# Kernel tuning notes

Measured on AMD Instinct MI355X. Metric: run time of the kernel, lower is better.

## Reference

```python
import jax, jax.numpy as jnp
import numpy as np

N_NODES = 50000
N_EDGES = 800000
D_IN = 128
D_HID = 128
D_OUT = 128
N_LAYERS = 2
NEG_SLOPE = 0.2


def leaky(x):
    return jnp.where(x >= 0, x, NEG_SLOPE * x)


def setup_inputs() -> dict:
    key = jax.random.key(0)
    ks = jax.random.split(key, 12)
    s = 1.0 / np.sqrt(D_HID)
    feats = jax.random.normal(ks[0], (N_NODES, D_IN), dtype=jnp.float32)
    src = jax.random.randint(ks[1], (N_EDGES,), 0, N_NODES)
    dst = jax.random.randint(ks[2], (N_EDGES,), 0, N_NODES)
    # SIRConv params per layer: W_Q (dst), W_K (src), W_R (output proj)
    Wq = jax.random.normal(ks[3], (N_LAYERS, D_IN, D_HID), dtype=jnp.float32) * s
    bq = jnp.zeros((N_LAYERS, D_HID), dtype=jnp.float32)
    Wk = jax.random.normal(ks[4], (N_LAYERS, D_IN, D_HID), dtype=jnp.float32) * s
    bk = jnp.zeros((N_LAYERS, D_HID), dtype=jnp.float32)
    Wr = jax.random.normal(ks[5], (N_LAYERS, D_HID, D_HID), dtype=jnp.float32) * s
    br = jnp.zeros((N_LAYERS, D_HID), dtype=jnp.float32)
    # Jumping-knowledge readouts: one per entry of feats_list (input + each layer);
    # input_dim == hidden_dim so weights stack along the leading axis.
    Wro = jax.random.normal(ks[6], (N_LAYERS + 1, D_HID, D_OUT), dtype=jnp.float32) * s
    bro = jnp.zeros((N_LAYERS + 1, D_OUT), dtype=jnp.float32)
    return {"feats": feats, "Wq": Wq, "bq": bq, "Wk": Wk, "bk": bk,
            "Wr": Wr, "br": br, "Wro": Wro, "bro": bro,
            "src": src, "dst": dst}


def reference(feats, Wq, bq, Wk, bk, Wr, br, Wro, bro, src, dst):
    # mean-aggregation denominator: in-degree, clamped to 1
    deg = jax.ops.segment_sum(jnp.ones((N_EDGES,), jnp.float32), dst,
                              num_segments=N_NODES)
    denom = jnp.maximum(deg, 1.0)[:, None]  # [N, 1]

    feats_list = [feats]
    h = feats
    for i in range(N_LAYERS):
        hq = h @ Wq[i] + bq[i]          # [N, H] (dst transform)
        hk = h @ Wk[i] + bk[i]          # [N, H] (src transform)
        m = leaky(hq[dst] + hk[src])    # [E, H] contextualized messages
        agg = jax.ops.segment_sum(m, dst, num_segments=N_NODES) / denom
        h = agg @ Wr[i] + br[i]         # conv output (+ residual = 0)
        h = leaky(h)                    # norm='none', dropout=0
        feats_list.append(h)

    # jumping-knowledge readout: sum of per-stage linear readouts
    score = feats_list[0] @ Wro[0] + bro[0]
    for i in range(1, N_LAYERS + 1):
        score = score + feats_list[i] @ Wro[i] + bro[i]
    return score
```

## Files before the change

kernel.cpp:

```cpp
#include <hip/hip_runtime.h>

#define NN 50000
#define NE 800000
#define D 128
#define NEG 0.2f

#define NBLK1 256
#define TILE1 3125
#define NB2 196
#define CAP2 8192
#define NT64 782

#define SB_PREP 576
#define SB_CONV 6250
#define SB_HIST NBLK1
#define SB_TOTAL (SB_PREP + SB_CONV + SB_HIST)

typedef short bf8_t __attribute__((ext_vector_type(8)));
typedef float f4_t __attribute__((ext_vector_type(4)));

__device__ __forceinline__ unsigned short f2bf(float f) {
  unsigned int u = __float_as_uint(f);
  return (unsigned short)((u + 0x7FFF + ((u >> 16) & 1)) >> 16);
}
__device__ __forceinline__ float bf2f(unsigned int b) { return __uint_as_float(b << 16); }

__device__ __forceinline__ f4_t MF(bf8_t a, bf8_t b, f4_t c) {
  return __builtin_amdgcn_mfma_f32_16x16x32_bf16(a, b, c, 0, 0, 0);
}

__device__ __forceinline__ int swz_u(int u) { return u ^ ((u >> 4) & 7); }


__device__ __forceinline__ void stage_wh(unsigned short* wbuf,
                                         const unsigned short* __restrict__ WTh, int t) {
#pragma unroll
  for (int i = 0; i < 4; ++i) {
    int u = t + i * 256;
    *(uint4*)(wbuf + swz_u(u) * 8) = *(const uint4*)(WTh + u * 8);
  }
}

__device__ __forceinline__ void load_a16(const unsigned short* __restrict__ A,
                                         int base, int l15, int quad, bf8_t (&afr)[4]) {
  int r = base + l15;
  if (r >= NN) r = NN - 1;
  const unsigned short* p = A + (size_t)r * D + quad * 8;
#pragma unroll
  for (int kc = 0; kc < 4; ++kc) afr[kc] = *(const bf8_t*)(p + kc * 32);
}

__device__ __forceinline__ void load_a16_lds(const unsigned short* buf, int wave,
                                             int l15, int quad, bf8_t (&afr)[4]) {
  const int r = wave * 16 + l15;
#pragma unroll
  for (int kc = 0; kc < 4; ++kc)
    afr[kc] = *(const bf8_t*)(buf + swz_u(r * 16 + kc * 4 + quad) * 8);
}

__device__ __forceinline__ void tile16h(const unsigned short* wbuf, const bf8_t (&afr)[4],
                                        int l15, int quad, f4_t* acc4) {
#pragma unroll
  for (int kc = 0; kc < 4; ++kc)
#pragma unroll
    for (int nt = 0; nt < 4; ++nt) {
      bf8_t b = *(const bf8_t*)(wbuf + swz_u((nt * 16 + l15) * 16 + kc * 4 + quad) * 8);
      acc4[nt] = MF(afr[kc], b, acc4[nt]);
    }
}

__device__ __forceinline__ void store_c8(unsigned short* __restrict__ C,
                                         const float* __restrict__ bias,
                                         const f4_t (&acc)[8], int base, int l15,
                                         int quad, bool lk) {
#pragma unroll
  for (int j = 0; j < 8; ++j) {
    int col = (j >> 2) * 64 + (j & 3) * 16 + l15;
    float bb = bias[col];
#pragma unroll
    for (int reg = 0; reg < 4; ++reg) {
      int row = base + quad * 4 + reg;
      if (row < NN) {
        float v = acc[j][reg] + bb;
        if (lk) v = v >= 0.f ? v : NEG * v;
        C[(size_t)row * D + col] = f2bf(v);
      }
    }
  }
}

#define ACC_TO_ABUF(ACC, BIAS)                                        \
  {                                                                   \
    _Pragma("unroll") for (int j = 0; j < 8; ++j) {                   \
      int col = (j >> 2) * 64 + (j & 3) * 16 + l15;                   \
      float bb = (BIAS)[col];                                         \
      _Pragma("unroll") for (int reg = 0; reg < 4; ++reg) {           \
        int rl = wave * 16 + quad * 4 + reg;                          \
        float v = ACC[j][reg] + bb;                                   \
        v = v >= 0.f ? v : NEG * v;                                   \
        int s = rl * D + col;                                         \
        abuf[s ^ ((rl & 7) << 3)] = f2bf(v);                          \
      }                                                               \
    }                                                                 \
  }

__global__ __launch_bounds__(256) void setup(
    const float* __restrict__ Wq, const float* __restrict__ Wk,
    const float* __restrict__ Wr, const float* __restrict__ Wro,
    const float* __restrict__ feats, const int* __restrict__ dst,
    unsigned short* __restrict__ WT, unsigned short* __restrict__ x0,
    int* __restrict__ H) {
  __shared__ int cnt[NB2];
  const int b = blockIdx.x;
  const int t = threadIdx.x;
  if (b < SB_PREP) {
    const int m = b >> 6, xb = b & 63;
    const float* src;
    if (m < 2) src = Wq + m * D * D;
    else if (m < 4) src = Wk + (m - 2) * D * D;
    else if (m < 6) src = Wr + (m - 4) * D * D;
    else src = Wro + (m - 6) * D * D;
    const int n = xb * 2 + (t >> 7);
    const int k = t & 127;
    WT[(size_t)m * D * D + n * D + k] = f2bf(src[k * D + n]);
  } else if (b < SB_PREP + SB_CONV) {
    int i = ((b - SB_PREP) * 256 + t) * 4;
    float4 v = *(const float4*)(feats + i);
    ushort4 o = {f2bf(v.x), f2bf(v.y), f2bf(v.z), f2bf(v.w)};
    *(ushort4*)(x0 + i) = o;
  } else {
    const int blk = b - SB_PREP - SB_CONV;
    if (t < NB2) cnt[t] = 0;
    __syncthreads();
    const int beg = blk * TILE1, end = beg + TILE1;
    for (int i = beg + t; i < end; i += 256) atomicAdd(&cnt[dst[i] >> 8], 1);
    __syncthreads();
    if (t < NB2) H[t * NBLK1 + blk] = cnt[t];
  }
}

__global__ __launch_bounds__(256) void p1_scan(const int* __restrict__ H,
                                               int* __restrict__ gofs) {
  __shared__ int sd[256];
  __shared__ int wsum[4];
  const int bin = blockIdx.x;
  const int t = threadIdx.x;
  const int wave = t >> 6, lane = t & 63;
  int part = 0;
  for (int b2 = 0; b2 < bin; ++b2) part += H[b2 * NBLK1 + t];
  for (int off = 32; off; off >>= 1) part += __shfl_down(part, off, 64);
  if (lane == 0) wsum[wave] = part;
  __syncthreads();
  const int base = wsum[0] + wsum[1] + wsum[2] + wsum[3];
  int x = H[bin * NBLK1 + t];
  sd[t] = x;
  __syncthreads();
  int acc = x;
  for (int off = 1; off < 256; off <<= 1) {
    int y = (t >= off) ? sd[t - off] : 0;
    __syncthreads();
    acc += y;
    sd[t] = acc;
    __syncthreads();
  }
  gofs[bin * NBLK1 + t] = base + (acc - x);
}

__global__ __launch_bounds__(256) void p1_scatter(const int* __restrict__ src,
                                                  const int* __restrict__ dst,
                                                  const int* __restrict__ gofs,
                                                  unsigned int* __restrict__ ebuf) {
  __shared__ int lofs[NB2];
  const int t = threadIdx.x;
  const int blk = blockIdx.x;
  if (t < NB2) lofs[t] = gofs[t * NBLK1 + blk];
  __syncthreads();
  const int beg = blk * TILE1, end = beg + TILE1;
  for (int i = beg + t; i < end; i += 256) {
    unsigned int d = (unsigned int)dst[i];
    int pos = atomicAdd(&lofs[d >> 8], 1);
    ebuf[pos] = (unsigned int)src[i] | (d << 16);
  }
}

__global__ __launch_bounds__(256) void sort_qk0(
    const int* __restrict__ gofs, const unsigned int* __restrict__ ebuf,
    int* __restrict__ ssrc, int* __restrict__ rowptr, int* __restrict__ deg,
    const unsigned short* __restrict__ x0,
    const unsigned short* __restrict__ WTq, const float* __restrict__ bq_,
    const unsigned short* __restrict__ WTk, const float* __restrict__ bk_,
    unsigned short* __restrict__ hq, unsigned short* __restrict__ hk) {
  __shared__ __align__(16) unsigned char smraw[35840];
  const int t = threadIdx.x;
  const int gx = blockIdx.x;
  if (gx < NB2) {
    int* cnt = (int*)smraw;
    int* fill = cnt + 256;
    int* sd = fill + 256;
    unsigned int* sorted = (unsigned int*)(sd + 256);
    const int b = gx;
    const int beg = gofs[b * NBLK1];
    const int end = (b + 1 < NB2) ? gofs[(b + 1) * NBLK1] : NE;
    const int n = end - beg;
    cnt[t] = 0;
    __syncthreads();
    for (int i = beg + t; i < end; i += 256)
      atomicAdd(&cnt[(ebuf[i] >> 16) & 255], 1);
    __syncthreads();
    int x = cnt[t];
    sd[t] = x;
    __syncthreads();
    int acc = x;
    for (int off = 1; off < 256; off <<= 1) {
      int y = (t >= off) ? sd[t - off] : 0;
      __syncthreads();
      acc += y;
      sd[t] = acc;
      __syncthreads();
    }
    const int excl = acc - x;
    fill[t] = excl;
    __syncthreads();
    for (int i = beg + t; i < end; i += 256) {
      unsigned int p = ebuf[i];
      int pos = atomicAdd(&fill[(p >> 16) & 255], 1);
      if (pos < CAP2) sorted[pos] = p;
    }
    __syncthreads();
    for (int i = t; i < n; i += 256) ssrc[beg + i] = (int)(sorted[i] & 0xFFFFu);
    const int node = (b << 8) + t;
    if (node < NN) {
      rowptr[node] = beg + excl;
      deg[node] = x;
    }
    if (b == 0 && t == 0) rowptr[NN] = NE;
  } else {
    unsigned short* wbuf = (unsigned short*)smraw;
    const int tile = gx - NB2;
    const int wave = t >> 6, lane = t & 63;
    const int l15 = lane & 15, quad = lane >> 4;
    const int base = tile * 64 + wave * 16;
    bf8_t afr[4];
    load_a16(x0, base, l15, quad, afr);
    stage_wh(wbuf, WTq, t);
    __syncthreads();
    f4_t aq[8] = {};
    tile16h(wbuf, afr, l15, quad, aq);
    __syncthreads();
    stage_wh(wbuf, WTq + 64 * D, t);
    __syncthreads();
    tile16h(wbuf, afr, l15, quad, aq + 4);
    store_c8(hq, bq_, aq, base, l15, quad, false);
    __syncthreads();
    stage_wh(wbuf, WTk, t);
    __syncthreads();
    f4_t ak[8] = {};
    tile16h(wbuf, afr, l15, quad, ak);
    __syncthreads();
    stage_wh(wbuf, WTk + 64 * D, t);
    __syncthreads();
    tile16h(wbuf, afr, l15, quad, ak + 4);
    store_c8(hk, bk_, ak, base, l15, quad, false);
  }
}

#define PROC(kb)                                                     \
  {                                                                  \
    float m;                                                         \
    m = q[0] + bf2f(kb.x & 0xFFFFu); a[0] += m >= 0.f ? m : NEG * m; \
    m = q[1] + bf2f(kb.x >> 16);     a[1] += m >= 0.f ? m : NEG * m; \
    m = q[2] + bf2f(kb.y & 0xFFFFu); a[2] += m >= 0.f ? m : NEG * m; \
    m = q[3] + bf2f(kb.y >> 16);     a[3] += m >= 0.f ? m : NEG * m; \
    m = q[4] + bf2f(kb.z & 0xFFFFu); a[4] += m >= 0.f ? m : NEG * m; \
    m = q[5] + bf2f(kb.z >> 16);     a[5] += m >= 0.f ? m : NEG * m; \
    m = q[6] + bf2f(kb.w & 0xFFFFu); a[6] += m >= 0.f ? m : NEG * m; \
    m = q[7] + bf2f(kb.w >> 16);     a[7] += m >= 0.f ? m : NEG * m; \
  }

__global__ __launch_bounds__(256) void aggregate(
    const int* __restrict__ rowptr, const int* __restrict__ ssrc,
    const int* __restrict__ deg,
    const unsigned short* __restrict__ hq, const unsigned short* __restrict__ hk,
    unsigned short* __restrict__ ag) {
  const int wave = threadIdx.x >> 6, lane = threadIdx.x & 63;
  const int v = blockIdx.x * 4 + wave;
  if (v >= NN) return;
  const int sub = lane & 15, grp = lane >> 4;
  const int beg = rowptr[v], end = rowptr[v + 1];

  uint4 qb = *(const uint4*)(hq + (size_t)v * D + sub * 8);
  float q[8];
  q[0] = bf2f(qb.x & 0xFFFFu); q[1] = bf2f(qb.x >> 16);
  q[2] = bf2f(qb.y & 0xFFFFu); q[3] = bf2f(qb.y >> 16);
  q[4] = bf2f(qb.z & 0xFFFFu); q[5] = bf2f(qb.z >> 16);
  q[6] = bf2f(qb.w & 0xFFFFu); q[7] = bf2f(qb.w >> 16);

  float a[8] = {0.f, 0.f, 0.f, 0.f, 0.f, 0.f, 0.f, 0.f};
  int e = beg + grp;
  for (; e + 12 < end; e += 16) {
    int s0 = ssrc[e];
    int s1 = ssrc[e + 4];
    int s2 = ssrc[e + 8];
    int s3 = ssrc[e + 12];
    uint4 k0 = *(const uint4*)(hk + (size_t)s0 * D + sub * 8);
    uint4 k1 = *(const uint4*)(hk + (size_t)s1 * D + sub * 8);
    uint4 k2 = *(const uint4*)(hk + (size_t)s2 * D + sub * 8);
    uint4 k3 = *(const uint4*)(hk + (size_t)s3 * D + sub * 8);
    PROC(k0);
    PROC(k1);
    PROC(k2);
    PROC(k3);
  }
  for (; e + 4 < end; e += 8) {
    int s0 = ssrc[e];
    int s1 = ssrc[e + 4];
    uint4 k0 = *(const uint4*)(hk + (size_t)s0 * D + sub * 8);
    uint4 k1 = *(const uint4*)(hk + (size_t)s1 * D + sub * 8);
    PROC(k0);
    PROC(k1);
  }
  if (e < end) {
    int s0 = ssrc[e];
    uint4 k0 = *(const uint4*)(hk + (size_t)s0 * D + sub * 8);
    PROC(k0);
  }
#pragma unroll
  for (int j = 0; j < 8; ++j) {
    a[j] += __shfl_xor(a[j], 16, 64);
    a[j] += __shfl_xor(a[j], 32, 64);
  }
  if (grp == 0) {
    float inv = 1.f / fmaxf((float)deg[v], 1.f);
    uint4 o;
    o.x = (unsigned int)f2bf(a[0] * inv) | ((unsigned int)f2bf(a[1] * inv) << 16);
    o.y = (unsigned int)f2bf(a[2] * inv) | ((unsigned int)f2bf(a[3] * inv) << 16);
    o.z = (unsigned int)f2bf(a[4] * inv) | ((unsigned int)f2bf(a[5] * inv) << 16);
    o.w = (unsigned int)f2bf(a[6] * inv) | ((unsigned int)f2bf(a[7] * inv) << 16);
    *(uint4*)(ag + (size_t)v * D + sub * 8) = o;
  }
}

__global__ __launch_bounds__(256) void wr_qk1(
    const unsigned short* __restrict__ ag,
    const unsigned short* __restrict__ WTr, const float* __restrict__ brr,
    unsigned short* __restrict__ h1,
    const unsigned short* __restrict__ WTq, const float* __restrict__ bq1,
    unsigned short* __restrict__ hq,
    const unsigned short* __restrict__ WTk, const float* __restrict__ bk1,
    unsigned short* __restrict__ hk) {
  __shared__ unsigned short wbuf[64 * D];
  __shared__ unsigned short abuf[64 * D];
  const int t = threadIdx.x, wave = t >> 6, lane = t & 63;
  const int l15 = lane & 15, quad = lane >> 4;
  const int tb = blockIdx.x * 64;
  const int base = tb + wave * 16;

  bf8_t afr[4];
  load_a16(ag, base, l15, quad, afr);
  stage_wh(wbuf, WTr, t);
  __syncthreads();
  f4_t acc[8] = {};
  tile16h(wbuf, afr, l15, quad, acc);
  __syncthreads();
  stage_wh(wbuf, WTr + 64 * D, t);
  __syncthreads();
  tile16h(wbuf, afr, l15, quad, acc + 4);

  ACC_TO_ABUF(acc, brr);
  __syncthreads();

  bf8_t hfr[4];
  load_a16_lds(abuf, wave, l15, quad, hfr);
#pragma unroll
  for (int i = 0; i < 4; ++i) {
    int u = t + i * 256;
    int row = tb + (u >> 4);
    if (row < NN)
      *(uint4*)(h1 + (size_t)tb * D + u * 8) = *(const uint4*)(abuf + swz_u(u) * 8);
  }

  stage_wh(wbuf, WTq, t);
  __syncthreads();
  f4_t aq[8] = {};
  tile16h(wbuf, hfr, l15, quad, aq);
  __syncthreads();
  stage_wh(wbuf, WTq + 64 * D, t);
  __syncthreads();
  tile16h(wbuf, hfr, l15, quad, aq + 4);
  store_c8(hq, bq1, aq, base, l15, quad, false);
  __syncthreads();

  stage_wh(wbuf, WTk, t);
  __syncthreads();
  f4_t ak[8] = {};
  tile16h(wbuf, hfr, l15, quad, ak);
  __syncthreads();
  stage_wh(wbuf, WTk + 64 * D, t);
  __syncthreads();
  tile16h(wbuf, hfr, l15, quad, ak + 4);
  store_c8(hk, bk1, ak, base, l15, quad, false);
}

__global__ __launch_bounds__(256) void wr_ro(
    const unsigned short* __restrict__ ag,
    const unsigned short* __restrict__ WTr, const float* __restrict__ brr,
    const unsigned short* __restrict__ x0,
    const unsigned short* __restrict__ h1,
    const unsigned short* __restrict__ WTro, const float* __restrict__ bro_,
    float* __restrict__ out) {
  __shared__ unsigned short wbuf[64 * D];
  __shared__ unsigned short abuf[64 * D];
  const int t = threadIdx.x, wave = t >> 6, lane = t & 63;
  const int l15 = lane & 15, quad = lane >> 4;
  const int tb = blockIdx.x * 64;
  const int base = tb + wave * 16;
  const size_t WM = (size_t)D * D;

  bf8_t afr[4];
  load_a16(ag, base, l15, quad, afr);
  stage_wh(wbuf, WTr, t);
  __syncthreads();
  f4_t acch[8] = {};
  tile16h(wbuf, afr, l15, quad, acch);
  __syncthreads();
  stage_wh(wbuf, WTr + 64 * D, t);
  __syncthreads();
  tile16h(wbuf, afr, l15, quad, acch + 4);

  ACC_TO_ABUF(acch, brr);
  __syncthreads();

  bf8_t hfr[4];
  load_a16_lds(abuf, wave, l15, quad, hfr);
  f4_t acc[8] = {};

  stage_wh(wbuf, WTro + 2 * WM, t);
  __syncthreads();
  tile16h(wbuf, hfr, l15, quad, acc);
  __syncthreads();
  stage_wh(wbuf, WTro + 2 * WM + 64 * D, t);
  __syncthreads();
  tile16h(wbuf, hfr, l15, quad, acc + 4);
  __syncthreads();

  load_a16(x0, base, l15, quad, afr);
  stage_wh(wbuf, WTro, t);
  __syncthreads();
  tile16h(wbuf, afr, l15, quad, acc);
  __syncthreads();
  stage_wh(wbuf, WTro + 64 * D, t);
  __syncthreads();
  tile16h(wbuf, afr, l15, quad, acc + 4);
  __syncthreads();

  load_a16(h1, base, l15, quad, afr);
  stage_wh(wbuf, WTro + WM, t);
  __syncthreads();
  tile16h(wbuf, afr, l15, quad, acc);
  __syncthreads();
  stage_wh(wbuf, WTro + WM + 64 * D, t);
  __syncthreads();
  tile16h(wbuf, afr, l15, quad, acc + 4);

#pragma unroll
  for (int j = 0; j < 8; ++j) {
    int col = (j >> 2) * 64 + (j & 3) * 16 + l15;
    float bsum = bro_[col] + bro_[D + col] + bro_[2 * D + col];
#pragma unroll
    for (int reg = 0; reg < 4; ++reg) {
      int row = base + quad * 4 + reg;
      if (row < NN) out[(size_t)row * D + col] = acc[j][reg] + bsum;
    }
  }
}

extern "C" void kernel_launch(void* const* d_in, const int* in_sizes, int n_in,
                              void* d_out, int out_size, void* d_ws, size_t ws_size,
                              hipStream_t stream) {
  const float* feats = (const float*)d_in[0];
  const float* Wq = (const float*)d_in[1];
  const float* bq = (const float*)d_in[2];
  const float* Wk = (const float*)d_in[3];
  const float* bk = (const float*)d_in[4];
  const float* Wr = (const float*)d_in[5];
  const float* br = (const float*)d_in[6];
  const float* Wro = (const float*)d_in[7];
  const float* bro = (const float*)d_in[8];
  const int* src = (const int*)d_in[9];
  const int* dst = (const int*)d_in[10];
  float* out = (float*)d_out;

  size_t off = 0;
  char* base = (char*)d_ws;
  auto alloc = [&](size_t bytes) -> void* {
    void* p = base + off;
    off += (bytes + 255) & ~(size_t)255;
    return p;
  };
  int* H = (int*)alloc((size_t)NB2 * NBLK1 * 4);
  int* gofs = (int*)alloc((size_t)NB2 * NBLK1 * 4);
  unsigned int* ebuf = (unsigned int*)alloc((size_t)NE * 4);
  int* ssrc = (int*)alloc((size_t)NE * 4);
  int* rowptr = (int*)alloc((size_t)(NN + 1) * 4);
  int* deg = (int*)alloc((size_t)NN * 4);
  unsigned short* WT = (unsigned short*)alloc((size_t)9 * D * D * 2);
  unsigned short* x0 = (unsigned short*)alloc((size_t)NN * D * 2);
  unsigned short* hq = (unsigned short*)alloc((size_t)NN * D * 2);
  unsigned short* hk = (unsigned short*)alloc((size_t)NN * D * 2);
  unsigned short* ag = (unsigned short*)alloc((size_t)NN * D * 2);
  unsigned short* h1 = (unsigned short*)alloc((size_t)NN * D * 2);

  const size_t WM = (size_t)D * D;
  const int ab = (NN + 3) / 4;

  setup<<<SB_TOTAL, 256, 0, stream>>>(Wq, Wk, Wr, Wro, feats, dst, WT, x0, H);
  p1_scan<<<NB2, 256, 0, stream>>>(H, gofs);
  p1_scatter<<<NBLK1, 256, 0, stream>>>(src, dst, gofs, ebuf);
  sort_qk0<<<NB2 + NT64, 256, 0, stream>>>(gofs, ebuf, ssrc, rowptr, deg,
                                           x0, WT + 0 * WM, bq, WT + 2 * WM, bk,
                                           hq, hk);
  aggregate<<<ab, 256, 0, stream>>>(rowptr, ssrc, deg, hq, hk, ag);
  wr_qk1<<<NT64, 256, 0, stream>>>(ag, WT + 4 * WM, br, h1,
                                   WT + 1 * WM, bq + D, hq,
                                   WT + 3 * WM, bk + D, hk);
  aggregate<<<ab, 256, 0, stream>>>(rowptr, ssrc, deg, hq, hk, ag);
  wr_ro<<<NT64, 256, 0, stream>>>(ag, WT + 5 * WM, br + D, x0, h1,
                                  WT + 6 * WM, bro, out);
}
```

Baseline: 281.8 us.

## Replace two-level bucket sort with global-atomic CSR build

Replaces the two-pass bucketed counting sort (block histograms, bin scan, bucket scatter, in-LDS per-bucket sort) with a simpler CSR build. In-degrees are counted with global atomics, a per-node prefix scan produces the row pointers, and edges are scattered with global atomics on per-node fill counters. This removes one kernel launch, the intermediate edge buffer and the LDS sort, in exchange for heavily contended global atomics and a non-deterministic order of edges within each row. It also adds a memset for the degree array.

```diff
diff --git a/kernel.cpp b/kernel.cpp
--- a/kernel.cpp
+++ b/kernel.cpp
@@ -5,16 +5,15 @@
 #define D 128
 #define NEG 0.2f
 
-#define NBLK1 256
 #define TILE1 3125
-#define NB2 196
-#define CAP2 8192
+#define SCB 196
+#define NSC 512
 #define NT64 782
 
 #define SB_PREP 576
 #define SB_CONV 6250
-#define SB_HIST NBLK1
-#define SB_TOTAL (SB_PREP + SB_CONV + SB_HIST)
+#define SB_EDGE 256
+#define SB_TOTAL (SB_PREP + SB_CONV + SB_EDGE)
 
 typedef short bf8_t __attribute__((ext_vector_type(8)));
 typedef float f4_t __attribute__((ext_vector_type(4)));
@@ -109,8 +108,7 @@
     const float* __restrict__ Wr, const float* __restrict__ Wro,
     const float* __restrict__ feats, const int* __restrict__ dst,
     unsigned short* __restrict__ WT, unsigned short* __restrict__ x0,
-    int* __restrict__ H) {
-  __shared__ int cnt[NB2];
+    int* __restrict__ deg) {
   const int b = blockIdx.x;
   const int t = threadIdx.x;
   if (b < SB_PREP) {
@@ -130,29 +128,27 @@
     *(ushort4*)(x0 + i) = o;
   } else {
     const int blk = b - SB_PREP - SB_CONV;
-    if (t < NB2) cnt[t] = 0;
-    __syncthreads();
     const int beg = blk * TILE1, end = beg + TILE1;
-    for (int i = beg + t; i < end; i += 256) atomicAdd(&cnt[dst[i] >> 8], 1);
-    __syncthreads();
-    if (t < NB2) H[t * NBLK1 + blk] = cnt[t];
-  }
-}
-
-__global__ __launch_bounds__(256) void p1_scan(const int* __restrict__ H,
-                                               int* __restrict__ gofs) {
+    for (int i = beg + t; i < end; i += 256) atomicAdd(&deg[dst[i]], 1);
+  }
+}
+
+__global__ __launch_bounds__(256) void scan(const int* __restrict__ deg,
+                                            int* __restrict__ rowptr,
+                                            int* __restrict__ fill) {
   __shared__ int sd[256];
   __shared__ int wsum[4];
-  const int bin = blockIdx.x;
+  const int b = blockIdx.x;
   const int t = threadIdx.x;
   const int wave = t >> 6, lane = t & 63;
   int part = 0;
-  for (int b2 = 0; b2 < bin; ++b2) part += H[b2 * NBLK1 + t];
+  for (int b2 = 0; b2 < b; ++b2) part += deg[b2 * 256 + t];
   for (int off = 32; off; off >>= 1) part += __shfl_down(part, off, 64);
   if (lane == 0) wsum[wave] = part;
   __syncthreads();
   const int base = wsum[0] + wsum[1] + wsum[2] + wsum[3];
-  int x = H[bin * NBLK1 + t];
+  const int g = b * 256 + t;
+  int x = (g < NN) ? deg[g] : 0;
   sd[t] = x;
   __syncthreads();
   int acc = x;
@@ -163,80 +159,33 @@
     sd[t] = acc;
     __syncthreads();
   }
-  gofs[bin * NBLK1 + t] = base + (acc - x);
-}
-
-__global__ __launch_bounds__(256) void p1_scatter(const int* __restrict__ src,
-                                                  const int* __restrict__ dst,
-                                                  const int* __restrict__ gofs,
-                                                  unsigned int* __restrict__ ebuf) {
-  __shared__ int lofs[NB2];
-  const int t = threadIdx.x;
-  const int blk = blockIdx.x;
-  if (t < NB2) lofs[t] = gofs[t * NBLK1 + blk];
-  __syncthreads();
-  const int beg = blk * TILE1, end = beg + TILE1;
-  for (int i = beg + t; i < end; i += 256) {
-    unsigned int d = (unsigned int)dst[i];
-    int pos = atomicAdd(&lofs[d >> 8], 1);
-    ebuf[pos] = (unsigned int)src[i] | (d << 16);
-  }
-}
-
-__global__ __launch_bounds__(256) void sort_qk0(
-    const int* __restrict__ gofs, const unsigned int* __restrict__ ebuf,
-    int* __restrict__ ssrc, int* __restrict__ rowptr, int* __restrict__ deg,
+  const int excl = base + acc - x;
+  if (g < NN) {
+    rowptr[g] = excl;
+    fill[g] = excl;
+  }
+  if (g == NN - 1) rowptr[NN] = excl + x;
+}
+
+__global__ __launch_bounds__(256) void scatter_qk0(
+    const int* __restrict__ src, const int* __restrict__ dst,
+    int* __restrict__ fill, int* __restrict__ ssrc,
     const unsigned short* __restrict__ x0,
     const unsigned short* __restrict__ WTq, const float* __restrict__ bq_,
     const unsigned short* __restrict__ WTk, const float* __restrict__ bk_,
     unsigned short* __restrict__ hq, unsigned short* __restrict__ hk) {
-  __shared__ __align__(16) unsigned char smraw[35840];
+  __shared__ unsigned short wbuf[64 * D];
   const int t = threadIdx.x;
   const int gx = blockIdx.x;
-  if (gx < NB2) {
-    int* cnt = (int*)smraw;
-    int* fill = cnt + 256;
-    int* sd = fill + 256;
-    unsigned int* sorted = (unsigned int*)(sd + 256);
-    const int b = gx;
-    const int beg = gofs[b * NBLK1];
-    const int end = (b + 1 < NB2) ? gofs[(b + 1) * NBLK1] : NE;
-    const int n = end - beg;
-    cnt[t] = 0;
-    __syncthreads();
-    for (int i = beg + t; i < end; i += 256)
-      atomicAdd(&cnt[(ebuf[i] >> 16) & 255], 1);
-    __syncthreads();
-    int x = cnt[t];
-    sd[t] = x;
-    __syncthreads();
-    int acc = x;
-    for (int off = 1; off < 256; off <<= 1) {
-      int y = (t >= off) ? sd[t - off] : 0;
-      __syncthreads();
-      acc += y;
-      sd[t] = acc;
-      __syncthreads();
+  if (gx < NSC) {
+    for (int i = gx * 256 + t; i < NE; i += NSC * 256) {
+      int d = dst[i];
+      int s = src[i];
+      int pos = atomicAdd(&fill[d], 1);
+      ssrc[pos] = s;
     }
-    const int excl = acc - x;
-    fill[t] = excl;
-    __syncthreads();
-    for (int i = beg + t; i < end; i += 256) {
-      unsigned int p = ebuf[i];
-      int pos = atomicAdd(&fill[(p >> 16) & 255], 1);
-      if (pos < CAP2) sorted[pos] = p;
-    }
-    __syncthreads();
-    for (int i = t; i < n; i += 256) ssrc[beg + i] = (int)(sorted[i] & 0xFFFFu);
-    const int node = (b << 8) + t;
-    if (node < NN) {
-      rowptr[node] = beg + excl;
-      deg[node] = x;
-    }
-    if (b == 0 && t == 0) rowptr[NN] = NE;
   } else {
-    unsigned short* wbuf = (unsigned short*)smraw;
-    const int tile = gx - NB2;
+    const int tile = gx - NSC;
     const int wave = t >> 6, lane = t & 63;
     const int l15 = lane & 15, quad = lane >> 4;
     const int base = tile * 64 + wave * 16;
@@ -497,12 +446,10 @@
     off += (bytes + 255) & ~(size_t)255;
     return p;
   };
-  int* H = (int*)alloc((size_t)NB2 * NBLK1 * 4);
-  int* gofs = (int*)alloc((size_t)NB2 * NBLK1 * 4);
-  unsigned int* ebuf = (unsigned int*)alloc((size_t)NE * 4);
+  int* deg = (int*)alloc((size_t)NN * 4);
+  int* rowptr = (int*)alloc((size_t)(NN + 1) * 4);
+  int* fill = (int*)alloc((size_t)NN * 4);
   int* ssrc = (int*)alloc((size_t)NE * 4);
-  int* rowptr = (int*)alloc((size_t)(NN + 1) * 4);
-  int* deg = (int*)alloc((size_t)NN * 4);
   unsigned short* WT = (unsigned short*)alloc((size_t)9 * D * D * 2);
   unsigned short* x0 = (unsigned short*)alloc((size_t)NN * D * 2);
   unsigned short* hq = (unsigned short*)alloc((size_t)NN * D * 2);
@@ -513,12 +460,12 @@
   const size_t WM = (size_t)D * D;
   const int ab = (NN + 3) / 4;
 
-  setup<<<SB_TOTAL, 256, 0, stream>>>(Wq, Wk, Wr, Wro, feats, dst, WT, x0, H);
-  p1_scan<<<NB2, 256, 0, stream>>>(H, gofs);
-  p1_scatter<<<NBLK1, 256, 0, stream>>>(src, dst, gofs, ebuf);
-  sort_qk0<<<NB2 + NT64, 256, 0, stream>>>(gofs, ebuf, ssrc, rowptr, deg,
-                                           x0, WT + 0 * WM, bq, WT + 2 * WM, bk,
-                                           hq, hk);
+  hipMemsetAsync(deg, 0, (size_t)NN * 4, stream);
+  setup<<<SB_TOTAL, 256, 0, stream>>>(Wq, Wk, Wr, Wro, feats, dst, WT, x0, deg);
+  scan<<<SCB, 256, 0, stream>>>(deg, rowptr, fill);
+  scatter_qk0<<<NSC + NT64, 256, 0, stream>>>(src, dst, fill, ssrc,
+                                              x0, WT + 0 * WM, bq, WT + 2 * WM, bk,
+                                              hq, hk);
   aggregate<<<ab, 256, 0, stream>>>(rowptr, ssrc, deg, hq, hk, ag);
   wr_qk1<<<NT64, 256, 0, stream>>>(ag, WT + 4 * WM, br, h1,
                                    WT + 1 * WM, bq + D, hq,
```

Result: slower. 362.2 us (+28.5%).

## Fuse bin-offset scan into scatter and sort directly into global CSR

Applied to the files above, without the earlier changes.

Removes the separate p1_scan kernel: each scatter block now reads a transposed histogram, computes per-bin totals and its own prefix, and does a wave-shuffle exclusive scan to get its local offsets. The per-bin sort no longer stages edges in a shared-memory buffer; it scatters source ids straight to global ssrc via shared atomic cursors. This cuts one launch, drops the barrier-heavy LDS scans, and shrinks shared memory, at the cost of every scatter block redundantly reading the full histogram and doing uncoalesced global writes.

```diff
diff --git a/kernel.cpp b/kernel.cpp
--- a/kernel.cpp
+++ b/kernel.cpp
@@ -8,7 +8,6 @@
 #define NBLK1 256
 #define TILE1 3125
 #define NB2 196
-#define CAP2 8192
 #define NT64 782
 
 #define SB_PREP 576
@@ -30,6 +29,21 @@
 }
 
 __device__ __forceinline__ int swz_u(int u) { return u ^ ((u >> 4) & 7); }
+
+__device__ __forceinline__ int excl_scan256(int x, int t, int* wsum) {
+  const int lane = t & 63, wave = t >> 6;
+  int v = x;
+#pragma unroll
+  for (int off = 1; off < 64; off <<= 1) {
+    int y = __shfl_up(v, off, 64);
+    if (lane >= off) v += y;
+  }
+  if (lane == 63) wsum[wave] = v;
+  __syncthreads();
+  int wbase = 0;
+  for (int w = 0; w < wave; ++w) wbase += wsum[w];
+  return wbase + v - x;
+}
 
 
 __device__ __forceinline__ void stage_wh(unsigned short* wbuf,
@@ -109,7 +123,7 @@
     const float* __restrict__ Wr, const float* __restrict__ Wro,
     const float* __restrict__ feats, const int* __restrict__ dst,
     unsigned short* __restrict__ WT, unsigned short* __restrict__ x0,
-    int* __restrict__ H) {
+    int* __restrict__ H_T) {
   __shared__ int cnt[NB2];
   const int b = blockIdx.x;
   const int t = threadIdx.x;
@@ -135,45 +149,30 @@
     const int beg = blk * TILE1, end = beg + TILE1;
     for (int i = beg + t; i < end; i += 256) atomicAdd(&cnt[dst[i] >> 8], 1);
     __syncthreads();
-    if (t < NB2) H[t * NBLK1 + blk] = cnt[t];
-  }
-}
-
-__global__ __launch_bounds__(256) void p1_scan(const int* __restrict__ H,
-                                               int* __restrict__ gofs) {
-  __shared__ int sd[256];
+    if (t < NB2) H_T[blk * NB2 + t] = cnt[t];
+  }
+}
+
+__global__ __launch_bounds__(256) void p1_scatter(
+    const int* __restrict__ src, const int* __restrict__ dst,
+    const int* __restrict__ H_T, int* __restrict__ bofs,
+    unsigned int* __restrict__ ebuf) {
+  __shared__ int lofs[NB2];
   __shared__ int wsum[4];
-  const int bin = blockIdx.x;
-  const int t = threadIdx.x;
-  const int wave = t >> 6, lane = t & 63;
-  int part = 0;
-  for (int b2 = 0; b2 < bin; ++b2) part += H[b2 * NBLK1 + t];
-  for (int off = 32; off; off >>= 1) part += __shfl_down(part, off, 64);
-  if (lane == 0) wsum[wave] = part;
-  __syncthreads();
-  const int base = wsum[0] + wsum[1] + wsum[2] + wsum[3];
-  int x = H[bin * NBLK1 + t];
-  sd[t] = x;
-  __syncthreads();
-  int acc = x;
-  for (int off = 1; off < 256; off <<= 1) {
-    int y = (t >= off) ? sd[t - off] : 0;
-    __syncthreads();
-    acc += y;
-    sd[t] = acc;
-    __syncthreads();
-  }
-  gofs[bin * NBLK1 + t] = base + (acc - x);
-}
-
-__global__ __launch_bounds__(256) void p1_scatter(const int* __restrict__ src,
-                                                  const int* __restrict__ dst,
-                                                  const int* __restrict__ gofs,
-                                                  unsigned int* __restrict__ ebuf) {
-  __shared__ int lofs[NB2];
   const int t = threadIdx.x;
   const int blk = blockIdx.x;
-  if (t < NB2) lofs[t] = gofs[t * NBLK1 + blk];
+  int total = 0, pref = 0;
+#pragma unroll 4
+  for (int j = 0; j < NBLK1; ++j) {
+    int h = (t < NB2) ? H_T[j * NB2 + t] : 0;
+    total += h;
+    if (j < blk) pref += h;
+  }
+  const int excl = excl_scan256(total, t, wsum);
+  if (t < NB2) {
+    lofs[t] = excl + pref;
+    if (blk == 0) bofs[t] = excl;
+  }
   __syncthreads();
   const int beg = blk * TILE1, end = beg + TILE1;
   for (int i = beg + t; i < end; i += 256) {
@@ -184,56 +183,42 @@
 }
 
 __global__ __launch_bounds__(256) void sort_qk0(
-    const int* __restrict__ gofs, const unsigned int* __restrict__ ebuf,
+    const int* __restrict__ bofs, const unsigned int* __restrict__ ebuf,
     int* __restrict__ ssrc, int* __restrict__ rowptr, int* __restrict__ deg,
     const unsigned short* __restrict__ x0,
     const unsigned short* __restrict__ WTq, const float* __restrict__ bq_,
     const unsigned short* __restrict__ WTk, const float* __restrict__ bk_,
     unsigned short* __restrict__ hq, unsigned short* __restrict__ hk) {
-  __shared__ __align__(16) unsigned char smraw[35840];
+  __shared__ __align__(16) unsigned char smraw[16384];
   const int t = threadIdx.x;
   const int gx = blockIdx.x;
   if (gx < NB2) {
     int* cnt = (int*)smraw;
     int* fill = cnt + 256;
-    int* sd = fill + 256;
-    unsigned int* sorted = (unsigned int*)(sd + 256);
+    int* wsum = fill + 256;
     const int b = gx;
-    const int beg = gofs[b * NBLK1];
-    const int end = (b + 1 < NB2) ? gofs[(b + 1) * NBLK1] : NE;
-    const int n = end - beg;
+    const int beg = bofs[b];
+    const int end = (b + 1 < NB2) ? bofs[b + 1] : NE;
     cnt[t] = 0;
     __syncthreads();
     for (int i = beg + t; i < end; i += 256)
       atomicAdd(&cnt[(ebuf[i] >> 16) & 255], 1);
     __syncthreads();
-    int x = cnt[t];
-    sd[t] = x;
-    __syncthreads();
-    int acc = x;
-    for (int off = 1; off < 256; off <<= 1) {
-      int y = (t >= off) ? sd[t - off] : 0;
-      __syncthreads();
-      acc += y;
-      sd[t] = acc;
-      __syncthreads();
-    }
-    const int excl = acc - x;
-    fill[t] = excl;
-    __syncthreads();
-    for (int i = beg + t; i < end; i += 256) {
-      unsigned int p = ebuf[i];
-      int pos = atomicAdd(&fill[(p >> 16) & 255], 1);
-      if (pos < CAP2) sorted[pos] = p;
-    }
-    __syncthreads();
-    for (int i = t; i < n; i += 256) ssrc[beg + i] = (int)(sorted[i] & 0xFFFFu);
+    const int x = cnt[t];
+    const int excl = excl_scan256(x, t, wsum);
+    fill[t] = beg + excl;
     const int node = (b << 8) + t;
     if (node < NN) {
       rowptr[node] = beg + excl;
       deg[node] = x;
     }
     if (b == 0 && t == 0) rowptr[NN] = NE;
+    __syncthreads();
+    for (int i = beg + t; i < end; i += 256) {
+      unsigned int p = ebuf[i];
+      int pos = atomicAdd(&fill[(p >> 16) & 255], 1);
+      ssrc[pos] = (int)(p & 0xFFFFu);
+    }
   } else {
     unsigned short* wbuf = (unsigned short*)smraw;
     const int tile = gx - NB2;
@@ -497,8 +482,8 @@
     off += (bytes + 255) & ~(size_t)255;
     return p;
   };
-  int* H = (int*)alloc((size_t)NB2 * NBLK1 * 4);
-  int* gofs = (int*)alloc((size_t)NB2 * NBLK1 * 4);
+  int* H_T = (int*)alloc((size_t)NBLK1 * NB2 * 4);
+  int* bofs = (int*)alloc((size_t)NB2 * 4);
   unsigned int* ebuf = (unsigned int*)alloc((size_t)NE * 4);
   int* ssrc = (int*)alloc((size_t)NE * 4);
   int* rowptr = (int*)alloc((size_t)(NN + 1) * 4);
@@ -513,10 +498,9 @@
   const size_t WM = (size_t)D * D;
   const int ab = (NN + 3) / 4;
 
-  setup<<<SB_TOTAL, 256, 0, stream>>>(Wq, Wk, Wr, Wro, feats, dst, WT, x0, H);
-  p1_scan<<<NB2, 256, 0, stream>>>(H, gofs);
-  p1_scatter<<<NBLK1, 256, 0, stream>>>(src, dst, gofs, ebuf);
-  sort_qk0<<<NB2 + NT64, 256, 0, stream>>>(gofs, ebuf, ssrc, rowptr, deg,
+  setup<<<SB_TOTAL, 256, 0, stream>>>(Wq, Wk, Wr, Wro, feats, dst, WT, x0, H_T);
+  p1_scatter<<<NBLK1, 256, 0, stream>>>(src, dst, H_T, bofs, ebuf);
+  sort_qk0<<<NB2 + NT64, 256, 0, stream>>>(bofs, ebuf, ssrc, rowptr, deg,
                                            x0, WT + 0 * WM, bq, WT + 2 * WM, bk,
                                            hq, hk);
   aggregate<<<ab, 256, 0, stream>>>(rowptr, ssrc, deg, hq, hk, ag);
```

Result: no change. 280.2 us (-0.6%).
